# Performance work log

Measured on AMD Instinct MI355X. Metric: run time of the kernel, lower is better.

The kernel has to match this reference:

```python
import jax, jax.numpy as jnp
import numpy as np

OUT = (7, 7, 7)      # output_size (D_out, H_out, W_out)
SCALE = 1.0          # spatial_scale


def setup_inputs() -> dict:
    key = jax.random.key(0)
    k1, k2 = jax.random.split(key)
    B, C, D, H, W = 2, 256, 64, 64, 64
    N = 512
    features = jax.random.normal(k1, (B, C, D, H, W), dtype=jnp.float32)
    p = jax.random.uniform(k2, (B, N, 6), dtype=jnp.float32) * 63.0
    lo = jnp.minimum(p[..., :3], p[..., 3:])
    hi = jnp.maximum(p[..., :3], p[..., 3:])
    proposals = jnp.concatenate([lo, hi], axis=-1)  # (B, N, 6) valid boxes
    return {"features": features, "proposals": proposals}


def _trilinear(vol, gz, gy, gx):
    # vol: (C, D, H, W); gz/gy/gx: (Do, Ho, Wo) voxel-space coords.
    # grid_sample(mode='bilinear', padding_mode='zeros', align_corners=True)
    C, D, H, W = vol.shape
    z0f, y0f, x0f = jnp.floor(gz), jnp.floor(gy), jnp.floor(gx)
    wz, wy, wx = gz - z0f, gy - y0f, gx - x0f
    z0, y0, x0 = z0f.astype(jnp.int32), y0f.astype(jnp.int32), x0f.astype(jnp.int32)

    def gather(zi, yi, xi):
        valid = (zi >= 0) & (zi < D) & (yi >= 0) & (yi < H) & (xi >= 0) & (xi < W)
        v = vol[:, jnp.clip(zi, 0, D - 1), jnp.clip(yi, 0, H - 1), jnp.clip(xi, 0, W - 1)]
        return v * valid.astype(vol.dtype)[None]  # (C, Do, Ho, Wo)

    out = jnp.zeros((C,) + gz.shape, dtype=vol.dtype)
    for dz in (0, 1):
        for dy in (0, 1):
            for dx in (0, 1):
                w = ((wz if dz else 1.0 - wz)
                     * (wy if dy else 1.0 - wy)
                     * (wx if dx else 1.0 - wx))
                out = out + gather(z0 + dz, y0 + dy, x0 + dx) * w[None]
    return out


def reference(features, proposals):
    # features: (B, C, D, H, W); proposals: (B, N, 6) [x1,y1,z1,x2,y2,z2]
    B, C, D, H, W = features.shape
    Do, Ho, Wo = OUT

    def one_roi(vol, prop):
        p = prop * SCALE
        x1, y1, z1, x2, y2, z2 = p[0], p[1], p[2], p[3], p[4], p[5]
        zc = jnp.linspace(z1, z2, Do)
        yc = jnp.linspace(y1, y2, Ho)
        xc = jnp.linspace(x1, x2, Wo)
        gz, gy, gx = jnp.meshgrid(zc, yc, xc, indexing='ij')  # (Do,Ho,Wo)
        return _trilinear(vol, gz, gy, gx)  # (C, Do, Ho, Wo)

    per_batch = jax.vmap(lambda vol, props: jax.vmap(lambda p: one_roi(vol, p))(props))
    out = per_batch(features, proposals)  # (B, N, C, Do, Ho, Wo)
    return out.reshape(B * proposals.shape[1], C, Do, Ho, Wo)
```

## Files before the change

kernel.cpp:

```cpp
#include <hip/hip_runtime.h>
#include <hip/hip_fp16.h>


#define B_      2
#define C_      256
#define N_      512
#define NENT    (N_ * 7)
#define SP      66
#define PLANE_P (64 * SP)
#define THREADS 1024
#define GROUPS  20
#define REC_F_BASE 128
#define WS_NEEDED ((size_t)REC_F_BASE * 4 + (size_t)B_ * NENT * 8 * 4)

typedef _Float16 h2v __attribute__((ext_vector_type(2)));

__device__ __forceinline__ float gcoord(float lo, float hi, int i) {
    return lo + (hi - lo) * (1.0f / 6.0f) * (float)i;
}

__device__ __forceinline__ uint32_t pkrtz(float a, float b) {
    auto h = __builtin_amdgcn_cvt_pkrtz(a, b);
    return __builtin_bit_cast(uint32_t, h);
}

__device__ __forceinline__ float xlerp(uint32_t pkv, uint32_t pkw) {
#if __has_builtin(__builtin_amdgcn_fdot2)
    return __builtin_amdgcn_fdot2(__builtin_bit_cast(h2v, pkv),
                                  __builtin_bit_cast(h2v, pkw), 0.0f, false);
#else
    h2v v = __builtin_bit_cast(h2v, pkv);
    h2v w = __builtin_bit_cast(h2v, pkw);
    return (float)v[0] * (float)w[0] + (float)v[1] * (float)w[1];
#endif
}

__global__ __launch_bounds__(256) void bucket_kernel(
    const float* __restrict__ props, int* __restrict__ wsi, float* __restrict__ wsf)
{
    int b = blockIdx.x;
    __shared__ int counts[63];
    __shared__ int starts[64];
    __shared__ int cursors[63];
    int tid = threadIdx.x;
    if (tid < 63) counts[tid] = 0;
    __syncthreads();
    for (int e = tid; e < NENT; e += 256) {
        int n = e / 7, iz = e - n * 7;
        const float* pr = props + (size_t)(b * N_ + n) * 6;
        float gz = gcoord(pr[2], pr[5], iz);
        int z0 = min(max((int)gz, 0), 62);
        atomicAdd(&counts[z0], 1);
    }
    __syncthreads();
    if (tid == 0) {
        int s = 0;
        for (int k = 0; k < 63; ++k) { starts[k] = s; s += counts[k]; }
        starts[63] = s;
    }
    __syncthreads();
    if (tid < 63) cursors[tid] = starts[tid];
    __syncthreads();
    for (int e = tid; e < NENT; e += 256) {
        int n = e / 7, iz = e - n * 7;
        const float* pr = props + (size_t)(b * N_ + n) * 6;
        float x1p = pr[0], y1p = pr[1], z1p = pr[2];
        float x2p = pr[3], y2p = pr[4], z2p = pr[5];
        float gz = gcoord(z1p, z2p, iz);
        int z0 = min(max((int)gz, 0), 62);
        float wz = gz - (float)z0;
        int pos = atomicAdd(&cursors[z0], 1);
        int off = (b * N_ + n) * (C_ * 343) + iz * 49;
        float* r = wsf + REC_F_BASE + (size_t)(b * NENT + pos) * 8;
        r[0] = x1p; r[1] = (x2p - x1p) * (1.0f / 6.0f);
        r[2] = y1p; r[3] = (y2p - y1p) * (1.0f / 6.0f);
        r[4] = wz;  r[5] = __int_as_float(off);
        r[6] = 0.0f; r[7] = 0.0f;
    }
    if (tid < 64) wsi[b * 64 + tid] = starts[tid];
}

__global__ __launch_bounds__(THREADS, 8) void roialign3d_zpair_kernel(
    const float* __restrict__ feat,
    const int* __restrict__ wsi,
    const float* __restrict__ wsf,
    float* __restrict__ out)
{
    __shared__ __align__(16) uint2 pk2[2 * PLANE_P];

    int bid = blockIdx.x;
    int pi  = bid & 255;
    int z0  = bid >> 8;
    int b   = pi >> 7;
    int c0  = (pi & 127) << 1;
    int tid = threadIdx.x;

    int base = wsi[b * 64 + z0];
    int end  = wsi[b * 64 + z0 + 1];
    if (base == end) return;

    const float* vol0 = feat + ((size_t)((b << 8) + c0) << 18) + ((size_t)z0 << 12);
    const float* vol1 = vol0 + (1 << 18);

    float4 a0 = *(const float4*)(vol0 + (tid << 2));
    float4 a1 = *(const float4*)(vol0 + 4096 + (tid << 2));
    float4 b0 = *(const float4*)(vol1 + (tid << 2));
    float4 b1 = *(const float4*)(vol1 + 4096 + (tid << 2));

    int g = tid / 49;
    int p = tid - g * 49;
    int iy = p / 7;
    float fx = (float)(p - iy * 7);
    float fy = (float)iy;
    const float4* recs = (const float4*)(wsf + REC_F_BASE);
    const int rbase = b * NENT;
    int myEnd = (g < GROUPS) ? end : base;
    int e = base + g;
    float4 rA, rB, rAn, rBn;
    if (e < myEnd) {
        rA = recs[(size_t)(rbase + e) * 2];
        rB = recs[(size_t)(rbase + e) * 2 + 1];
        if (e + GROUPS < myEnd) {
            rAn = recs[(size_t)(rbase + e + GROUPS) * 2];
            rBn = recs[(size_t)(rbase + e + GROUPS) * 2 + 1];
        }
    }

    {
        int swb = (tid >> 4) * SP + ((tid & 15) << 2);
        float a0n = __shfl_down(a0.x, 1);
        float a1n = __shfl_down(a1.x, 1);
        float b0n = __shfl_down(b0.x, 1);
        float b1n = __shfl_down(b1.x, 1);
        uint2* d0 = &pk2[swb];
        uint2* d1 = &pk2[PLANE_P + swb];
        d0[0] = make_uint2(pkrtz(a0.x, a0.y), pkrtz(a1.x, a1.y));
        d0[1] = make_uint2(pkrtz(a0.y, a0.z), pkrtz(a1.y, a1.z));
        d0[2] = make_uint2(pkrtz(a0.z, a0.w), pkrtz(a1.z, a1.w));
        d0[3] = make_uint2(pkrtz(a0.w, a0n),  pkrtz(a1.w, a1n));
        d1[0] = make_uint2(pkrtz(b0.x, b0.y), pkrtz(b1.x, b1.y));
        d1[1] = make_uint2(pkrtz(b0.y, b0.z), pkrtz(b1.y, b1.z));
        d1[2] = make_uint2(pkrtz(b0.z, b0.w), pkrtz(b1.z, b1.w));
        d1[3] = make_uint2(pkrtz(b0.w, b0n),  pkrtz(b1.w, b1n));
    }
    __syncthreads();

    float* outc = out + (size_t)c0 * 343;
    while (e < myEnd) {
        float gx = fmaf(rA.y, fx, rA.x);
        float gy = fmaf(rA.w, fy, rA.z);
        int x0 = (int)gx, y0 = (int)gy;
        float wx = __builtin_amdgcn_fractf(gx);
        float wy = __builtin_amdgcn_fractf(gy);
        uint32_t pw = pkrtz(1.0f - wx, wx);
        float wz = rB.x;
        int offc = __float_as_int(rB.y);
        int sl = y0 * SP + x0;
        uint2 qa0 = pk2[sl],           qa1 = pk2[sl + SP];
        uint2 qb0 = pk2[PLANE_P + sl], qb1 = pk2[PLANE_P + sl + SP];

        float4 tA = rAn, tB = rBn;
        int e2 = e + 2 * GROUPS;
        if (e2 < myEnd) {
            rAn = recs[(size_t)(rbase + e2) * 2];
            rBn = recs[(size_t)(rbase + e2) * 2 + 1];
        }

        {
            float c00 = xlerp(qa0.x, pw);
            float c10 = xlerp(qa0.y, pw);
            float c01 = xlerp(qa1.x, pw);
            float c11 = xlerp(qa1.y, pw);
            float d0 = fmaf(c01 - c00, wy, c00);
            float d1 = fmaf(c11 - c10, wy, c10);
            outc[offc + p] = fmaf(d1 - d0, wz, d0);
        }
        {
            float c00 = xlerp(qb0.x, pw);
            float c10 = xlerp(qb0.y, pw);
            float c01 = xlerp(qb1.x, pw);
            float c11 = xlerp(qb1.y, pw);
            float d0 = fmaf(c01 - c00, wy, c00);
            float d1 = fmaf(c11 - c10, wy, c10);
            outc[offc + 343 + p] = fmaf(d1 - d0, wz, d0);
        }

        e += GROUPS; rA = tA; rB = tB;
    }
}

__global__ __launch_bounds__(128) void roialign3d_fallback(
    const float* __restrict__ feat, const float* __restrict__ props,
    float* __restrict__ out)
{
    int bid = blockIdx.x;
    int xcd = bid & 7;
    int j   = bid >> 3;
    int s   = xcd + ((j >> 9) << 3);
    int n   = j & 511;
    int b   = s >> 8;
    int c   = s & 255;
    const float* prop = props + ((size_t)(b * N_ + n)) * 6;
    float x1p = prop[0], y1p = prop[1], z1p = prop[2];
    float x2p = prop[3], y2p = prop[4], z2p = prop[5];
    float sx = (x2p - x1p) * (1.0f / 6.0f);
    float sy = (y2p - y1p) * (1.0f / 6.0f);
    float sz = (z2p - z1p) * (1.0f / 6.0f);
    const float* vol = feat + (size_t)s * (64 * 64 * 64);
    float* o = out + ((size_t)(b * N_ + n) * C_ + c) * 343;
    for (int p = threadIdx.x; p < 343; p += 128) {
        int iz = p / 49, r = p - iz * 49, iy = r / 7, ix = r - iy * 7;
        float gx = x1p + sx * ix, gy = y1p + sy * iy, gz = z1p + sz * iz;
        int x0 = (int)gx, y0 = (int)gy, z0 = (int)gz;
        float wx = gx - x0, wy = gy - y0, wz = gz - z0;
        int x1 = min(x0 + 1, 63), y1 = min(y0 + 1, 63), z1 = min(z0 + 1, 63);
        const float* p00 = vol + ((z0 * 64 + y0) << 6);
        const float* p01 = vol + ((z0 * 64 + y1) << 6);
        const float* p10 = vol + ((z1 * 64 + y0) << 6);
        const float* p11 = vol + ((z1 * 64 + y1) << 6);
        float c00 = p00[x0] + (p00[x1] - p00[x0]) * wx;
        float c01 = p01[x0] + (p01[x1] - p01[x0]) * wx;
        float c10 = p10[x0] + (p10[x1] - p10[x0]) * wx;
        float c11 = p11[x0] + (p11[x1] - p11[x0]) * wx;
        float d0 = c00 + (c01 - c00) * wy;
        float d1 = c10 + (c11 - c10) * wy;
        o[p] = d0 + (d1 - d0) * wz;
    }
}

extern "C" void kernel_launch(void* const* d_in, const int* in_sizes, int n_in,
                              void* d_out, int out_size, void* d_ws, size_t ws_size,
                              hipStream_t stream) {
    const float* feat  = (const float*)d_in[0];
    const float* props = (const float*)d_in[1];
    float* out = (float*)d_out;

    if (ws_size < WS_NEEDED) {
        roialign3d_fallback<<<B_ * C_ * N_, 128, 0, stream>>>(feat, props, out);
        return;
    }
    int*   wsi = (int*)d_ws;
    float* wsf = (float*)d_ws;
    bucket_kernel<<<B_, 256, 0, stream>>>(props, wsi, wsf);
    roialign3d_zpair_kernel<<<63 * 256, THREADS, 0, stream>>>(feat, wsi, wsf, out);
}
```

Baseline: 300.0 us.

## Split channel-pair blocks into single-channel 512-thread blocks with 8-wide staging

Each block now handles one (batch, channel, z-slice) instead of a channel pair. Block size drops to 512 threads with 10 entry groups, and the grid doubles to 63*512 blocks. The shared-memory plane halves, and each thread loads 8 contiguous floats per row to build packed fp16 x-pairs with 16-byte LDS stores. The aim is higher occupancy and finer scheduling granularity, at the cost of more blocks, re-reading the bucket records per channel, and fewer groups per block to amortize staging.

```diff
diff --git a/kernel.cpp b/kernel.cpp
--- a/kernel.cpp
+++ b/kernel.cpp
@@ -7,9 +7,8 @@
 #define N_      512
 #define NENT    (N_ * 7)
 #define SP      66
-#define PLANE_P (64 * SP)
-#define THREADS 1024
-#define GROUPS  20
+#define THREADS 512
+#define GROUPS  10
 #define REC_F_BASE 128
 #define WS_NEEDED ((size_t)REC_F_BASE * 4 + (size_t)B_ * NENT * 8 * 4)
 
@@ -80,32 +79,34 @@
     if (tid < 64) wsi[b * 64 + tid] = starts[tid];
 }
 
-__global__ __launch_bounds__(THREADS, 8) void roialign3d_zpair_kernel(
+__global__ __launch_bounds__(THREADS, 8) void roialign3d_small_kernel(
     const float* __restrict__ feat,
     const int* __restrict__ wsi,
     const float* __restrict__ wsf,
     float* __restrict__ out)
 {
-    __shared__ __align__(16) uint2 pk2[2 * PLANE_P];
+    __shared__ __align__(16) uint2 pk2[64 * SP];
 
     int bid = blockIdx.x;
-    int pi  = bid & 255;
-    int z0  = bid >> 8;
-    int b   = pi >> 7;
-    int c0  = (pi & 127) << 1;
+    int s   = bid & 511;
+    int z0  = bid >> 9;
+    int b   = s >> 8;
+    int c   = s & 255;
     int tid = threadIdx.x;
 
     int base = wsi[b * 64 + z0];
     int end  = wsi[b * 64 + z0 + 1];
     if (base == end) return;
 
-    const float* vol0 = feat + ((size_t)((b << 8) + c0) << 18) + ((size_t)z0 << 12);
-    const float* vol1 = vol0 + (1 << 18);
-
-    float4 a0 = *(const float4*)(vol0 + (tid << 2));
-    float4 a1 = *(const float4*)(vol0 + 4096 + (tid << 2));
-    float4 b0 = *(const float4*)(vol1 + (tid << 2));
-    float4 b1 = *(const float4*)(vol1 + 4096 + (tid << 2));
+    const float* vol = feat + ((size_t)s << 18) + ((size_t)z0 << 12);
+
+    int y  = tid >> 3;
+    int x8 = (tid & 7) << 3;
+    const float* src = vol + y * 64 + x8;
+    float4 p0a = *(const float4*)(src);
+    float4 p0b = *(const float4*)(src + 4);
+    float4 p1a = *(const float4*)(src + 4096);
+    float4 p1b = *(const float4*)(src + 4100);
 
     int g = tid / 49;
     int p = tid - g * 49;
@@ -127,25 +128,23 @@
     }
 
     {
-        int swb = (tid >> 4) * SP + ((tid & 15) << 2);
-        float a0n = __shfl_down(a0.x, 1);
-        float a1n = __shfl_down(a1.x, 1);
-        float b0n = __shfl_down(b0.x, 1);
-        float b1n = __shfl_down(b1.x, 1);
-        uint2* d0 = &pk2[swb];
-        uint2* d1 = &pk2[PLANE_P + swb];
-        d0[0] = make_uint2(pkrtz(a0.x, a0.y), pkrtz(a1.x, a1.y));
-        d0[1] = make_uint2(pkrtz(a0.y, a0.z), pkrtz(a1.y, a1.z));
-        d0[2] = make_uint2(pkrtz(a0.z, a0.w), pkrtz(a1.z, a1.w));
-        d0[3] = make_uint2(pkrtz(a0.w, a0n),  pkrtz(a1.w, a1n));
-        d1[0] = make_uint2(pkrtz(b0.x, b0.y), pkrtz(b1.x, b1.y));
-        d1[1] = make_uint2(pkrtz(b0.y, b0.z), pkrtz(b1.y, b1.z));
-        d1[2] = make_uint2(pkrtz(b0.z, b0.w), pkrtz(b1.z, b1.w));
-        d1[3] = make_uint2(pkrtz(b0.w, b0n),  pkrtz(b1.w, b1n));
-    }
-    __syncthreads();
-
-    float* outc = out + (size_t)c0 * 343;
+        float n0 = __shfl_down(p0a.x, 1);
+        float n1 = __shfl_down(p1a.x, 1);
+        uint4* d = (uint4*)&pk2[y * SP + x8];
+        uint4 w0, w1, w2, w3;
+        w0.x = pkrtz(p0a.x, p0a.y); w0.y = pkrtz(p1a.x, p1a.y);
+        w0.z = pkrtz(p0a.y, p0a.z); w0.w = pkrtz(p1a.y, p1a.z);
+        w1.x = pkrtz(p0a.z, p0a.w); w1.y = pkrtz(p1a.z, p1a.w);
+        w1.z = pkrtz(p0a.w, p0b.x); w1.w = pkrtz(p1a.w, p1b.x);
+        w2.x = pkrtz(p0b.x, p0b.y); w2.y = pkrtz(p1b.x, p1b.y);
+        w2.z = pkrtz(p0b.y, p0b.z); w2.w = pkrtz(p1b.y, p1b.z);
+        w3.x = pkrtz(p0b.z, p0b.w); w3.y = pkrtz(p1b.z, p1b.w);
+        w3.z = pkrtz(p0b.w, n0);    w3.w = pkrtz(p1b.w, n1);
+        d[0] = w0; d[1] = w1; d[2] = w2; d[3] = w3;
+    }
+    __syncthreads();
+
+    float* outc = out + (size_t)c * 343;
     while (e < myEnd) {
         float gx = fmaf(rA.y, fx, rA.x);
         float gy = fmaf(rA.w, fy, rA.z);
@@ -156,8 +155,8 @@
         float wz = rB.x;
         int offc = __float_as_int(rB.y);
         int sl = y0 * SP + x0;
-        uint2 qa0 = pk2[sl],           qa1 = pk2[sl + SP];
-        uint2 qb0 = pk2[PLANE_P + sl], qb1 = pk2[PLANE_P + sl + SP];
+        uint2 q0 = pk2[sl];
+        uint2 q1 = pk2[sl + SP];
 
         float4 tA = rAn, tB = rBn;
         int e2 = e + 2 * GROUPS;
@@ -166,24 +165,13 @@
             rBn = recs[(size_t)(rbase + e2) * 2 + 1];
         }
 
-        {
-            float c00 = xlerp(qa0.x, pw);
-            float c10 = xlerp(qa0.y, pw);
-            float c01 = xlerp(qa1.x, pw);
-            float c11 = xlerp(qa1.y, pw);
-            float d0 = fmaf(c01 - c00, wy, c00);
-            float d1 = fmaf(c11 - c10, wy, c10);
-            outc[offc + p] = fmaf(d1 - d0, wz, d0);
-        }
-        {
-            float c00 = xlerp(qb0.x, pw);
-            float c10 = xlerp(qb0.y, pw);
-            float c01 = xlerp(qb1.x, pw);
-            float c11 = xlerp(qb1.y, pw);
-            float d0 = fmaf(c01 - c00, wy, c00);
-            float d1 = fmaf(c11 - c10, wy, c10);
-            outc[offc + 343 + p] = fmaf(d1 - d0, wz, d0);
-        }
+        float c00 = xlerp(q0.x, pw);
+        float c10 = xlerp(q0.y, pw);
+        float c01 = xlerp(q1.x, pw);
+        float c11 = xlerp(q1.y, pw);
+        float d0 = fmaf(c01 - c00, wy, c00);
+        float d1 = fmaf(c11 - c10, wy, c10);
+        outc[offc + p] = fmaf(d1 - d0, wz, d0);
 
         e += GROUPS; rA = tA; rB = tB;
     }
@@ -242,5 +230,5 @@
     int*   wsi = (int*)d_ws;
     float* wsf = (float*)d_ws;
     bucket_kernel<<<B_, 256, 0, stream>>>(props, wsi, wsf);
-    roialign3d_zpair_kernel<<<63 * 256, THREADS, 0, stream>>>(feat, wsi, wsf, out);
-}
+    roialign3d_small_kernel<<<63 * 512, THREADS, 0, stream>>>(feat, wsi, wsf, out);
+}
```

Result: no change. 301.4 us (+0.5%).
